# Kernel optimization log

Hardware: AMD Instinct MI355X
Metric: run time of the kernel (lower is better)

Reference implementation:

```python
import jax, jax.numpy as jnp
import numpy as np

NUM_EMBEDDINGS = 1024
EMBEDDING_DIM = 64
COMMIT_COST = 0.25


def setup_inputs() -> dict:
    key = jax.random.key(0)
    k1, k2 = jax.random.split(key)
    latent = jax.random.normal(k1, (32, EMBEDDING_DIM, 32, 32), dtype=jnp.float32)
    embedding_weight = jax.random.normal(k2, (NUM_EMBEDDINGS, EMBEDDING_DIM), dtype=jnp.float32)
    return {"latent": latent, "embedding_weight": embedding_weight}


def reference(latent, embedding_weight):
    # rearrange 'b n j d -> b j d n'; n == embedding_dim
    lat = jnp.transpose(latent, (0, 2, 3, 1))  # [b, j, d, n]
    flat = lat.reshape(-1, EMBEDDING_DIM)      # [T, D]
    # squared-euclidean distances [T, K]
    distances = (
        jnp.sum(flat ** 2, axis=1, keepdims=True)
        + jnp.sum(embedding_weight ** 2, axis=1)
        - 2.0 * flat @ embedding_weight.T
    )
    idx = jnp.argmin(distances, axis=1)                         # [T]
    encodings = jax.nn.one_hot(idx, NUM_EMBEDDINGS, dtype=flat.dtype)  # [T, K]
    quantized_flat = embedding_weight[idx]                      # gather == encodings @ W
    quantized = quantized_flat.reshape(lat.shape)               # [b, j, d, n]

    e_latent_loss = jnp.mean((jax.lax.stop_gradient(quantized) - lat) ** 2)
    loss = COMMIT_COST * e_latent_loss

    # straight-through estimator
    quantized_st = lat + jax.lax.stop_gradient(quantized - lat)

    avg_probs = jnp.mean(encodings, axis=0)
    perplexity = jnp.exp(-jnp.sum(avg_probs * jnp.log(avg_probs + 1e-10)))

    # rearrange back 'b j d n -> b n j d'
    quantized_out = jnp.transpose(quantized_st, (0, 3, 1, 2))
    return quantized_out, loss, perplexity, encodings, distances
```

## Files before the change

### kernel.cpp

```cpp
#include <hip/hip_runtime.h>
#include <cfloat>

#define T_TOTAL 32768
#define DIM 64
#define KCODES 1024

static constexpr long long OFF_Q    = 0;
static constexpr long long OFF_LOSS = 2097152;
static constexpr long long OFF_PERP = 2097153;
static constexpr long long OFF_ENC  = 2097154;
static constexpr long long OFF_DIST = 2097154LL + 33554432LL;


#define AS1 __attribute__((address_space(1)))
#define AS3 __attribute__((address_space(3)))

__device__ __forceinline__ void gld16(const float* g, float* l) {
    __builtin_amdgcn_global_load_lds((const AS1 unsigned int*)g,
                                     (AS3 unsigned int*)l, 16, 0, 0);
}

#define PHASE_SYNC(N) do {                                        \
    asm volatile("s_waitcnt vmcnt(" #N ")" ::: "memory");         \
    __builtin_amdgcn_s_barrier();                                 \
    __builtin_amdgcn_sched_barrier(0);                            \
} while (0)

__global__ __launch_bounds__(256) void vq_prep_kernel(const float* __restrict__ W,
                                                      float* __restrict__ ww,
                                                      float* __restrict__ WT,
                                                      float* __restrict__ out,
                                                      int* __restrict__ counts,
                                                      float* __restrict__ lossSum) {
    const int tid = threadIdx.x;
    const int b   = blockIdx.x;
    if (b < 256) {
        const int lane = tid & 63;
        const int code = b * 4 + (tid >> 6);
        float v = W[code * DIM + lane];
        float s = v * v;
        #pragma unroll
        for (int off = 32; off > 0; off >>= 1)
            s += __shfl_down(s, off, 64);
        if (lane == 0) ww[code] = s;
    } else if (b < 320) {
        const int n = b - 256;
        #pragma unroll
        for (int i = 0; i < 4; ++i) {
            int k = i * 256 + tid;
            WT[n * KCODES + k] = W[k * DIM + n];
        }
    } else if (b < 384) {
        float* __restrict__ enc = out + OFF_ENC;
        const float2 z2 = make_float2(0.f, 0.f);
        const int r0 = (b - 320) * 512 + tid * 2;
        const long long rb = (long long)r0 * KCODES;
        *(float2*)&enc[rb]               = z2;
        *(float2*)&enc[rb + 1022]        = z2;
        *(float2*)&enc[rb + 1024]        = z2;
        *(float2*)&enc[rb + 1024 + 1022] = z2;
    } else {
        #pragma unroll
        for (int i = 0; i < 4; ++i) counts[i * 256 + tid] = 0;
        if (tid == 0) lossSum[0] = 0.f;
    }
}

__global__ __launch_bounds__(512, 4) void vq_main_kernel(const float* __restrict__ lat,
                                                         const float* __restrict__ W,
                                                         const float* __restrict__ ww,
                                                         const float* __restrict__ WT,
                                                         float* __restrict__ out,
                                                         int* __restrict__ counts,
                                                         float* __restrict__ lossSum) {
    __shared__ float xT[64 * 64];
    __shared__ float wS[2][8 * 512];
    __shared__ float wwS[KCODES];
    __shared__ float xx[64];
    __shared__ int   selIdx[64];

    const int tid = threadIdx.x;
    const int tx  = tid & 63;
    const int ty  = tid >> 6;
    const int t0  = blockIdx.x * 64;
    const long long base = (long long)(t0 >> 10) * 65536 + (long long)(t0 & 1023);
    const int wbase = (tid & 448) * 4;

    #pragma unroll
    for (int i = 0; i < 2; ++i) {
        const int e = i * 512 + tid;
        gld16(&lat[base + (long long)(e >> 4) * 1024 + (e & 15) * 4],
              &xT[i * 2048 + wbase]);
    }
    #pragma unroll
    for (int i = 0; i < 2; ++i) {
        const int e = i * 512 + tid;
        gld16(&WT[(e >> 7) * KCODES + (e & 127) * 4],
              &wS[0][i * 2048 + wbase]);
    }
    *(float2*)&wwS[tid * 2] = *(const float2*)&ww[tid * 2];
    __syncthreads();

    if (tid < 64) {
        float s = 0.f;
        #pragma unroll 8
        for (int n = 0; n < 64; ++n) {
            float v = xT[n * 64 + tid];
            s = fmaf(v, v, s);
        }
        xx[tid] = s;
    }

    float minV[8];
    int   minI[8];
    #pragma unroll
    for (int r = 0; r < 8; ++r) { minV[r] = FLT_MAX; minI[r] = 0; }

    float acc[8][8];
    float* __restrict__ distOut = out + OFF_DIST;
    float* __restrict__ enc     = out + OFF_ENC;
    const float4 z4 = make_float4(0.f, 0.f, 0.f, 0.f);

    for (int p = 0; p < 16; ++p) {
        const int c   = p >> 3;
        const int q   = p & 7;
        const int buf = p & 1;

        if (p < 15) {
            const int pn = p + 1;
            const float* srcb = WT + (pn & 7) * (8 * KCODES) + (pn >> 3) * 512;
            float* dstb = &wS[pn & 1][0];
            #pragma unroll
            for (int i = 0; i < 2; ++i) {
                const int e = i * 512 + tid;
                gld16(&srcb[(e >> 7) * KCODES + (e & 127) * 4],
                      &dstb[i * 2048 + wbase]);
            }
        }
        asm volatile("" ::: "memory");

        {
            float4* pzf = (float4*)(enc + (long long)(t0 + p * 4) * KCODES + 2);
            const int rr = tid >> 7;
            const int j  = tid & 127;
            const int j2 = (j + 128 > 254) ? 254 : j + 128;
            pzf[rr * 256 + j]  = z4;
            pzf[rr * 256 + j2] = z4;
        }

        if (q == 0) {
            #pragma unroll
            for (int r = 0; r < 8; ++r)
                #pragma unroll
                for (int k = 0; k < 8; ++k) acc[r][k] = 0.f;
        }

        #pragma unroll 2
        for (int nn = 0; nn < 8; ++nn) {
            const float* xrow = &xT[(q * 8 + nn) * 64];
            const float* wrow = &wS[buf][nn * 512];
            float4 a0 = *(const float4*)&xrow[ty * 4];
            float4 a1 = *(const float4*)&xrow[32 + ty * 4];
            float4 b0 = *(const float4*)&wrow[tx * 4];
            float4 b1 = *(const float4*)&wrow[256 + tx * 4];
            float ar[8] = {a0.x, a0.y, a0.z, a0.w, a1.x, a1.y, a1.z, a1.w};
            float br[8] = {b0.x, b0.y, b0.z, b0.w, b1.x, b1.y, b1.z, b1.w};
            #pragma unroll
            for (int r = 0; r < 8; ++r)
                #pragma unroll
                for (int k = 0; k < 8; ++k)
                    acc[r][k] = fmaf(ar[r], br[k], acc[r][k]);
        }

        if (q == 7) {
            const int kb = c * 512 + tx * 4;
            float wr[8];
            {
                float4 wa = *(const float4*)&wwS[kb];
                float4 wb = *(const float4*)&wwS[kb + 256];
                wr[0]=wa.x; wr[1]=wa.y; wr[2]=wa.z; wr[3]=wa.w;
                wr[4]=wb.x; wr[5]=wb.y; wr[6]=wb.z; wr[7]=wb.w;
            }
            #pragma unroll
            for (int r = 0; r < 8; ++r) {
                const int row = (r >> 2) * 32 + ty * 4 + (r & 3);
                const float xxr = xx[row];
                const long long ro = (long long)(t0 + row) * KCODES + kb;
                #pragma unroll
                for (int g = 0; g < 2; ++g) {
                    float d0 = (xxr + wr[g*4+0]) - 2.f * acc[r][g*4+0];
                    float d1 = (xxr + wr[g*4+1]) - 2.f * acc[r][g*4+1];
                    float d2 = (xxr + wr[g*4+2]) - 2.f * acc[r][g*4+2];
                    float d3 = (xxr + wr[g*4+3]) - 2.f * acc[r][g*4+3];
                    const int k0 = kb + g * 256;
                    if (d0 < minV[r]) { minV[r] = d0; minI[r] = k0;     }
                    if (d1 < minV[r]) { minV[r] = d1; minI[r] = k0 + 1; }
                    if (d2 < minV[r]) { minV[r] = d2; minI[r] = k0 + 2; }
                    if (d3 < minV[r]) { minV[r] = d3; minI[r] = k0 + 3; }
                    *(float2*)&distOut[ro + g * 256]     = make_float2(d0, d1);
                    *(float2*)&distOut[ro + g * 256 + 2] = make_float2(d2, d3);
                }
            }
        }

        if (q == 7) PHASE_SYNC(34);
        else        PHASE_SYNC(2);
    }

    #pragma unroll
    for (int r = 0; r < 8; ++r) {
        float v  = minV[r];
        int   bi = minI[r];
        #pragma unroll
        for (int off = 1; off < 64; off <<= 1) {
            float v2 = __shfl_xor(v, off, 64);
            int   i2 = __shfl_xor(bi, off, 64);
            if (v2 < v || (v2 == v && i2 < bi)) { v = v2; bi = i2; }
        }
        if (tx == r) {
            const int row = (r >> 2) * 32 + ty * 4 + (r & 3);
            selIdx[row] = bi;
            atomicAdd(&counts[bi], 1);
        }
    }
    __syncthreads();

    float* qS = &wS[0][0];
    #pragma unroll
    for (int i = 0; i < 8; ++i) {
        int e   = i * 512 + tid;
        int row = e >> 6;
        int n   = e & 63;
        qS[row * 65 + n] = W[selIdx[row] * DIM + n];
    }
    __syncthreads();

    float ls = 0.f;
    #pragma unroll
    for (int i = 0; i < 2; ++i) {
        int e2  = i * 512 + tid;
        int n   = e2 >> 4;
        int tl0 = (e2 & 15) * 4;
        float q0 = qS[(tl0 + 0) * 65 + n];
        float q1 = qS[(tl0 + 1) * 65 + n];
        float q2 = qS[(tl0 + 2) * 65 + n];
        float q3 = qS[(tl0 + 3) * 65 + n];
        float x0 = xT[n * 64 + tl0 + 0];
        float x1 = xT[n * 64 + tl0 + 1];
        float x2 = xT[n * 64 + tl0 + 2];
        float x3 = xT[n * 64 + tl0 + 3];
        *(float4*)&out[OFF_Q + base + (long long)n * 1024 + tl0] = make_float4(q0, q1, q2, q3);
        float e0 = q0 - x0; ls = fmaf(e0, e0, ls);
        float e1 = q1 - x1; ls = fmaf(e1, e1, ls);
        float e2d = q2 - x2; ls = fmaf(e2d, e2d, ls);
        float e3 = q3 - x3; ls = fmaf(e3, e3, ls);
    }
    #pragma unroll
    for (int off = 32; off > 0; off >>= 1)
        ls += __shfl_down(ls, off, 64);
    if (tx == 0) atomicAdd(lossSum, ls);

    if (tid < 64)
        enc[(long long)(t0 + tid) * KCODES + selIdx[tid]] = 1.f;
}

__global__ __launch_bounds__(1024) void vq_finalize_kernel(const int* __restrict__ counts,
                                                           const float* __restrict__ lossSum,
                                                           float* __restrict__ out) {
    __shared__ float red[16];
    const int tid = threadIdx.x;
    float p = (float)counts[tid] * (1.0f / 32768.0f);
    float term = p * logf(p + 1e-10f);
    #pragma unroll
    for (int off = 32; off > 0; off >>= 1)
        term += __shfl_down(term, off, 64);
    if ((tid & 63) == 0) red[tid >> 6] = term;
    __syncthreads();
    if (tid == 0) {
        float s = 0.f;
        #pragma unroll
        for (int i = 0; i < 16; ++i) s += red[i];
        out[OFF_PERP] = expf(-s);
        out[OFF_LOSS] = 0.25f * lossSum[0] * (1.0f / 2097152.0f);
    }
}

extern "C" void kernel_launch(void* const* d_in, const int* in_sizes, int n_in,
                              void* d_out, int out_size, void* d_ws, size_t ws_size,
                              hipStream_t stream) {
    (void)in_sizes; (void)n_in; (void)out_size; (void)ws_size;
    const float* lat = (const float*)d_in[0];
    const float* W   = (const float*)d_in[1];
    float* out = (float*)d_out;

    int*   counts  = (int*)d_ws;
    float* ww      = (float*)((char*)d_ws + 4096);
    float* lossSum = (float*)((char*)d_ws + 8192);
    float* WT      = (float*)((char*)d_ws + 12288);

    vq_prep_kernel<<<385, 256, 0, stream>>>(W, ww, WT, out, counts, lossSum);
    vq_main_kernel<<<512, 512, 0, stream>>>(lat, W, ww, WT, out, counts, lossSum);
    vq_finalize_kernel<<<1, 1024, 0, stream>>>(counts, lossSum, out);
}
```

Baseline: 401.7 us.

## Stage full codebook half in LDS and use nontemporal stores for outputs

The main kernel previously streamed the codebook through a double-buffered 8-row LDS ring, with a barrier every phase. It now loads a whole 64x512 half of the transposed codebook into LDS at once, runs the full 64-deep dot product, then reloads the second half, which cuts the barrier count to a few. Output writes for distances, the one-hot zeroing and the quantized tensor switch to nontemporal stores to avoid cache pollution, and the row mapping per thread is changed to contiguous rows. The LDS footprint grows to about 150KB, so occupancy drops to one block per CU (launch bounds changed to 512,1), and the second-half load is only overlapped with the encoding stores and epilogue.

```diff
diff --git a/kernel.cpp b/kernel.cpp
--- a/kernel.cpp
+++ b/kernel.cpp
@@ -15,16 +15,26 @@
 #define AS1 __attribute__((address_space(1)))
 #define AS3 __attribute__((address_space(3)))
 
+typedef float __attribute__((ext_vector_type(2))) f32x2;
+typedef float __attribute__((ext_vector_type(4))) f32x4;
+
+__device__ __forceinline__ void ntstore2(float* p, float a, float b) {
+    f32x2 v = {a, b};
+    __builtin_nontemporal_store(v, (f32x2*)p);
+}
+__device__ __forceinline__ void ntstore4z(float* p) {
+    f32x4 v = {0.f, 0.f, 0.f, 0.f};
+    __builtin_nontemporal_store(v, (f32x4*)p);
+}
+__device__ __forceinline__ void ntstore4(float* p, float a, float b, float c, float d) {
+    f32x4 v = {a, b, c, d};
+    __builtin_nontemporal_store(v, (f32x4*)p);
+}
+
 __device__ __forceinline__ void gld16(const float* g, float* l) {
     __builtin_amdgcn_global_load_lds((const AS1 unsigned int*)g,
                                      (AS3 unsigned int*)l, 16, 0, 0);
 }
-
-#define PHASE_SYNC(N) do {                                        \
-    asm volatile("s_waitcnt vmcnt(" #N ")" ::: "memory");         \
-    __builtin_amdgcn_s_barrier();                                 \
-    __builtin_amdgcn_sched_barrier(0);                            \
-} while (0)
 
 __global__ __launch_bounds__(256) void vq_prep_kernel(const float* __restrict__ W,
                                                       float* __restrict__ ww,
@@ -52,13 +62,12 @@
         }
     } else if (b < 384) {
         float* __restrict__ enc = out + OFF_ENC;
-        const float2 z2 = make_float2(0.f, 0.f);
         const int r0 = (b - 320) * 512 + tid * 2;
         const long long rb = (long long)r0 * KCODES;
-        *(float2*)&enc[rb]               = z2;
-        *(float2*)&enc[rb + 1022]        = z2;
-        *(float2*)&enc[rb + 1024]        = z2;
-        *(float2*)&enc[rb + 1024 + 1022] = z2;
+        ntstore2(&enc[rb], 0.f, 0.f);
+        ntstore2(&enc[rb + 1022], 0.f, 0.f);
+        ntstore2(&enc[rb + 1024], 0.f, 0.f);
+        ntstore2(&enc[rb + 1024 + 1022], 0.f, 0.f);
     } else {
         #pragma unroll
         for (int i = 0; i < 4; ++i) counts[i * 256 + tid] = 0;
@@ -66,7 +75,7 @@
     }
 }
 
-__global__ __launch_bounds__(512, 4) void vq_main_kernel(const float* __restrict__ lat,
+__global__ __launch_bounds__(512, 1) void vq_main_kernel(const float* __restrict__ lat,
                                                          const float* __restrict__ W,
                                                          const float* __restrict__ ww,
                                                          const float* __restrict__ WT,
@@ -74,7 +83,7 @@
                                                          int* __restrict__ counts,
                                                          float* __restrict__ lossSum) {
     __shared__ float xT[64 * 64];
-    __shared__ float wS[2][8 * 512];
+    __shared__ float wC[64 * 512];
     __shared__ float wwS[KCODES];
     __shared__ float xx[64];
     __shared__ int   selIdx[64];
@@ -93,10 +102,10 @@
               &xT[i * 2048 + wbase]);
     }
     #pragma unroll
-    for (int i = 0; i < 2; ++i) {
+    for (int i = 0; i < 16; ++i) {
         const int e = i * 512 + tid;
         gld16(&WT[(e >> 7) * KCODES + (e & 127) * 4],
-              &wS[0][i * 2048 + wbase]);
+              &wC[i * 2048 + wbase]);
     }
     *(float2*)&wwS[tid * 2] = *(const float2*)&ww[tid * 2];
     __syncthreads();
@@ -119,48 +128,20 @@
     float acc[8][8];
     float* __restrict__ distOut = out + OFF_DIST;
     float* __restrict__ enc     = out + OFF_ENC;
-    const float4 z4 = make_float4(0.f, 0.f, 0.f, 0.f);
-
-    for (int p = 0; p < 16; ++p) {
-        const int c   = p >> 3;
-        const int q   = p & 7;
-        const int buf = p & 1;
-
-        if (p < 15) {
-            const int pn = p + 1;
-            const float* srcb = WT + (pn & 7) * (8 * KCODES) + (pn >> 3) * 512;
-            float* dstb = &wS[pn & 1][0];
-            #pragma unroll
-            for (int i = 0; i < 2; ++i) {
-                const int e = i * 512 + tid;
-                gld16(&srcb[(e >> 7) * KCODES + (e & 127) * 4],
-                      &dstb[i * 2048 + wbase]);
-            }
-        }
-        asm volatile("" ::: "memory");
-
-        {
-            float4* pzf = (float4*)(enc + (long long)(t0 + p * 4) * KCODES + 2);
-            const int rr = tid >> 7;
-            const int j  = tid & 127;
-            const int j2 = (j + 128 > 254) ? 254 : j + 128;
-            pzf[rr * 256 + j]  = z4;
-            pzf[rr * 256 + j2] = z4;
-        }
-
-        if (q == 0) {
-            #pragma unroll
-            for (int r = 0; r < 8; ++r)
-                #pragma unroll
-                for (int k = 0; k < 8; ++k) acc[r][k] = 0.f;
-        }
-
-        #pragma unroll 2
-        for (int nn = 0; nn < 8; ++nn) {
-            const float* xrow = &xT[(q * 8 + nn) * 64];
-            const float* wrow = &wS[buf][nn * 512];
-            float4 a0 = *(const float4*)&xrow[ty * 4];
-            float4 a1 = *(const float4*)&xrow[32 + ty * 4];
+
+    #pragma unroll 1
+    for (int c = 0; c < 2; ++c) {
+        #pragma unroll
+        for (int r = 0; r < 8; ++r)
+            #pragma unroll
+            for (int k = 0; k < 8; ++k) acc[r][k] = 0.f;
+
+        #pragma unroll 4
+        for (int n = 0; n < 64; ++n) {
+            const float* xrow = &xT[n * 64 + ty * 8];
+            const float* wrow = &wC[n * 512];
+            float4 a0 = *(const float4*)&xrow[0];
+            float4 a1 = *(const float4*)&xrow[4];
             float4 b0 = *(const float4*)&wrow[tx * 4];
             float4 b1 = *(const float4*)&wrow[256 + tx * 4];
             float ar[8] = {a0.x, a0.y, a0.z, a0.w, a1.x, a1.y, a1.z, a1.w};
@@ -172,39 +153,67 @@
                     acc[r][k] = fmaf(ar[r], br[k], acc[r][k]);
         }
 
-        if (q == 7) {
-            const int kb = c * 512 + tx * 4;
+        asm volatile("s_waitcnt lgkmcnt(0)" ::: "memory");
+        __builtin_amdgcn_s_barrier();
+        __builtin_amdgcn_sched_barrier(0);
+
+        if (c == 0) {
+            #pragma unroll
+            for (int i = 0; i < 16; ++i) {
+                const int e = i * 512 + tid;
+                gld16(&WT[(e >> 7) * KCODES + 512 + (e & 127) * 4],
+                      &wC[i * 2048 + wbase]);
+            }
+        }
+        asm volatile("" ::: "memory");
+
+        {
+            float* encBase = enc + (long long)(t0 + c * 32) * KCODES + 2;
+            #pragma unroll
+            for (int i = 0; i < 16; ++i) {
+                const int e   = i * 512 + tid;
+                const int row = e >> 8;
+                const int j   = e & 255;
+                const int jc  = j > 254 ? 254 : j;
+                ntstore4z(encBase + (long long)row * KCODES + jc * 4);
+            }
+        }
+        asm volatile("" ::: "memory");
+
+        {
+            const int kbl = tx * 4;
             float wr[8];
-            {
-                float4 wa = *(const float4*)&wwS[kb];
-                float4 wb = *(const float4*)&wwS[kb + 256];
-                wr[0]=wa.x; wr[1]=wa.y; wr[2]=wa.z; wr[3]=wa.w;
-                wr[4]=wb.x; wr[5]=wb.y; wr[6]=wb.z; wr[7]=wb.w;
-            }
+            float4 wa = *(const float4*)&wwS[c * 512 + kbl];
+            float4 wb = *(const float4*)&wwS[c * 512 + 256 + kbl];
+            wr[0]=wa.x; wr[1]=wa.y; wr[2]=wa.z; wr[3]=wa.w;
+            wr[4]=wb.x; wr[5]=wb.y; wr[6]=wb.z; wr[7]=wb.w;
             #pragma unroll
             for (int r = 0; r < 8; ++r) {
-                const int row = (r >> 2) * 32 + ty * 4 + (r & 3);
+                const int row = ty * 8 + r;
                 const float xxr = xx[row];
-                const long long ro = (long long)(t0 + row) * KCODES + kb;
+                const long long ro = (long long)(t0 + row) * KCODES + c * 512 + kbl;
                 #pragma unroll
                 for (int g = 0; g < 2; ++g) {
                     float d0 = (xxr + wr[g*4+0]) - 2.f * acc[r][g*4+0];
                     float d1 = (xxr + wr[g*4+1]) - 2.f * acc[r][g*4+1];
                     float d2 = (xxr + wr[g*4+2]) - 2.f * acc[r][g*4+2];
                     float d3 = (xxr + wr[g*4+3]) - 2.f * acc[r][g*4+3];
-                    const int k0 = kb + g * 256;
+                    const int k0 = c * 512 + g * 256 + kbl;
                     if (d0 < minV[r]) { minV[r] = d0; minI[r] = k0;     }
                     if (d1 < minV[r]) { minV[r] = d1; minI[r] = k0 + 1; }
                     if (d2 < minV[r]) { minV[r] = d2; minI[r] = k0 + 2; }
                     if (d3 < minV[r]) { minV[r] = d3; minI[r] = k0 + 3; }
-                    *(float2*)&distOut[ro + g * 256]     = make_float2(d0, d1);
-                    *(float2*)&distOut[ro + g * 256 + 2] = make_float2(d2, d3);
+                    ntstore2(&distOut[ro + g * 256],     d0, d1);
+                    ntstore2(&distOut[ro + g * 256 + 2], d2, d3);
                 }
             }
         }
 
-        if (q == 7) PHASE_SYNC(34);
-        else        PHASE_SYNC(2);
+        if (c == 0) {
+            asm volatile("s_waitcnt vmcnt(32)" ::: "memory");
+            __builtin_amdgcn_s_barrier();
+            __builtin_amdgcn_sched_barrier(0);
+        }
     }
 
     #pragma unroll
@@ -218,14 +227,13 @@
             if (v2 < v || (v2 == v && i2 < bi)) { v = v2; bi = i2; }
         }
         if (tx == r) {
-            const int row = (r >> 2) * 32 + ty * 4 + (r & 3);
-            selIdx[row] = bi;
+            selIdx[ty * 8 + r] = bi;
             atomicAdd(&counts[bi], 1);
         }
     }
     __syncthreads();
 
-    float* qS = &wS[0][0];
+    float* qS = wC;
     #pragma unroll
     for (int i = 0; i < 8; ++i) {
         int e   = i * 512 + tid;
@@ -249,7 +257,7 @@
         float x1 = xT[n * 64 + tl0 + 1];
         float x2 = xT[n * 64 + tl0 + 2];
         float x3 = xT[n * 64 + tl0 + 3];
-        *(float4*)&out[OFF_Q + base + (long long)n * 1024 + tl0] = make_float4(q0, q1, q2, q3);
+        ntstore4(&out[OFF_Q + base + (long long)n * 1024 + tl0], q0, q1, q2, q3);
         float e0 = q0 - x0; ls = fmaf(e0, e0, ls);
         float e1 = q1 - x1; ls = fmaf(e1, e1, ls);
         float e2d = q2 - x2; ls = fmaf(e2d, e2d, ls);
@@ -258,7 +266,7 @@
     #pragma unroll
     for (int off = 32; off > 0; off >>= 1)
         ls += __shfl_down(ls, off, 64);
-    if (tx == 0) atomicAdd(lossSum, ls);
+    if ((tid & 63) == 0) atomicAdd(lossSum, ls);
 
     if (tid < 64)
         enc[(long long)(t0 + tid) * KCODES + selIdx[tid]] = 1.f;
```

New measurement: 356.7 us. -11.2%, faster.
